# Optimization experiments

Hardware: AMD Instinct MI355X
Metric: run time of the kernel (lower is better)

## Reference

```python
import jax, jax.numpy as jnp
import numpy as np

N_EMBD = 1024
N_HEAD = 16
HEAD_DIM = N_EMBD // N_HEAD


def setup_inputs() -> dict:
    key = jax.random.key(0)
    k1, k2, k3 = jax.random.split(key, 3)
    x = jax.random.normal(k1, (4, 2048, N_EMBD), dtype=jnp.float32)
    w_qkv = jax.random.normal(k2, (N_EMBD, 3 * N_EMBD), dtype=jnp.float32) * (N_EMBD ** -0.5)
    w_proj = jax.random.normal(k3, (N_EMBD, N_EMBD), dtype=jnp.float32) * (N_EMBD ** -0.5)
    return {"x": x, "w_qkv": w_qkv, "w_proj": w_proj}


def reference(x, w_qkv, w_proj):
    B, T, C = x.shape
    qkv = jnp.einsum('btc,cd->btd', x, w_qkv)  # [B,T,3C]
    q, k, v = jnp.split(qkv, 3, axis=-1)
    def heads(t):
        return t.reshape(B, T, N_HEAD, HEAD_DIM).transpose(0, 2, 1, 3)  # [B,H,T,D]
    q, k, v = heads(q), heads(k), heads(v)
    scale = 1.0 / jnp.sqrt(jnp.asarray(HEAD_DIM, dtype=x.dtype))
    att = jnp.einsum('bhqd,bhkd->bhqk', q, k) * scale  # [B,H,T,T]
    causal = jnp.tril(jnp.ones((T, T), dtype=bool))
    att = jnp.where(causal[None, None], att, jnp.asarray(-jnp.inf, dtype=att.dtype))
    att = jax.nn.softmax(att, axis=-1)
    out = jnp.einsum('bhqk,bhkd->bhqd', att, v)  # [B,H,T,D]
    out = out.transpose(0, 2, 1, 3).reshape(B, T, C)
    return jnp.einsum('btc,cd->btd', out, w_proj)
```

## Files before the change

kernel.cpp:

```cpp
#include <hip/hip_runtime.h>
#include <cstdint>
#include <cstddef>
#include <type_traits>

typedef float  f32x4    __attribute__((ext_vector_type(4)));
typedef float  f32x16   __attribute__((ext_vector_type(16)));
typedef __bf16 bf16x8   __attribute__((ext_vector_type(8)));
typedef short  short4_t __attribute__((ext_vector_type(4)));
typedef short  short8_t __attribute__((ext_vector_type(8)));
typedef unsigned int uint4_t __attribute__((ext_vector_type(4)));

__device__ __forceinline__ short f2bf(float f) {
  return __builtin_bit_cast(short, (__bf16)f);
}

__device__ __forceinline__ unsigned pk2bf(float a, float b) {
  unsigned lo = (unsigned short)__builtin_bit_cast(unsigned short, f2bf(a));
  unsigned hi = (unsigned short)__builtin_bit_cast(unsigned short, f2bf(b));
  return lo | (hi << 16);
}

__device__ __forceinline__ void gl_lds16(const void* g, void* l) {
  __builtin_amdgcn_global_load_lds((const __attribute__((address_space(1))) void*)g,
                                   (__attribute__((address_space(3))) void*)l, 16, 0, 0);
}

__global__ void convert_bf16(const float* __restrict__ X, short* __restrict__ Xb) {
  int i = (blockIdx.x * 256 + threadIdx.x) * 4;
  f32x4 v = *(const f32x4*)&X[i];
  short4_t o;
#pragma unroll
  for (int j = 0; j < 4; j++) o[j] = f2bf(v[j]);
  *(short4_t*)&Xb[i] = o;
}

__global__ void transpose_bf16(const float* __restrict__ W, short* __restrict__ WT,
                               int K, int N) {
  __shared__ float tile[32][33];
  int tx = threadIdx.x & 31, ty = threadIdx.x >> 5;
  int n0 = blockIdx.x * 32, k0 = blockIdx.y * 32;
#pragma unroll
  for (int i = 0; i < 32; i += 8)
    tile[ty + i][tx] = W[(size_t)(k0 + ty + i) * N + n0 + tx];
  __syncthreads();
#pragma unroll
  for (int i = 0; i < 32; i += 8)
    WT[(size_t)(n0 + ty + i) * K + k0 + tx] = f2bf(tile[tx][ty + i]);
}

template <int MODE>
__global__ __launch_bounds__(256, 2) void gemm_bt(
    const short* __restrict__ A, const short* __restrict__ Bt,
    float* __restrict__ outf, short* __restrict__ Qo, short* __restrict__ Ko,
    short* __restrict__ Vo, int M, int N, int K) {
  __shared__ alignas(16) short As[128 * 32];
  __shared__ alignas(16) short Bs[128 * 32];
  const int tid = threadIdx.x;
  const int lane = tid & 63;
  const int g = lane & 15, q = lane >> 4;
  const int wave = tid >> 6;
  const int m0 = blockIdx.y * 128, n0 = blockIdx.x * 128;
  const int wm = (wave >> 1) * 64, wn = (wave & 1) * 64;

  const int srow = tid >> 2;
  const int scol = (tid & 3) * 8;
  const short* ap0 = A  + (size_t)(m0 + srow) * K + scol;
  const short* ap1 = A  + (size_t)(m0 + 64 + srow) * K + scol;
  const short* bp0 = Bt + (size_t)(n0 + srow) * K + scol;
  const short* bp1 = Bt + (size_t)(n0 + 64 + srow) * K + scol;
  short* la0 = &As[tid * 8];
  short* la1 = &As[(tid + 256) * 8];
  short* lb0 = &Bs[tid * 8];
  short* lb1 = &Bs[(tid + 256) * 8];

  f32x4 acc[4][4] = {};

  for (int k0 = 0; k0 < K; k0 += 32) {
    __syncthreads();
    gl_lds16(ap0 + k0, la0);
    gl_lds16(ap1 + k0, la1);
    gl_lds16(bp0 + k0, lb0);
    gl_lds16(bp1 + k0, lb1);
    __syncthreads();
    bf16x8 af[4], bfr[4];
#pragma unroll
    for (int mt = 0; mt < 4; mt++)
      af[mt] = *(const bf16x8*)&As[(wm + mt * 16 + g) * 32 + q * 8];
#pragma unroll
    for (int nt = 0; nt < 4; nt++)
      bfr[nt] = *(const bf16x8*)&Bs[(wn + nt * 16 + g) * 32 + q * 8];
#pragma unroll
    for (int mt = 0; mt < 4; mt++)
#pragma unroll
      for (int nt = 0; nt < 4; nt++)
        acc[mt][nt] = __builtin_amdgcn_mfma_f32_16x16x32_bf16(af[mt], bfr[nt],
                                                              acc[mt][nt], 0, 0, 0);
  }

  if (MODE == 0) {
#pragma unroll
    for (int mt = 0; mt < 4; mt++)
#pragma unroll
      for (int nt = 0; nt < 4; nt++) {
        int n = n0 + wn + nt * 16 + g;
        int mbase = m0 + wm + mt * 16 + q * 4;
#pragma unroll
        for (int r = 0; r < 4; r++)
          outf[(size_t)(mbase + r) * N + n] = acc[mt][nt][r];
      }
  } else {
#pragma unroll
    for (int nt = 0; nt < 4; nt++) {
      int n = n0 + wn + nt * 16 + g;
      int which = n >> 10;
      int c = n & 1023;
      int h = c >> 6, d = c & 63;
#pragma unroll
      for (int mt = 0; mt < 4; mt++) {
        int mbase = m0 + wm + mt * 16 + q * 4;
        int b = mbase >> 11, t = mbase & 2047;
        if (which == 2) {
          short4_t pv;
#pragma unroll
          for (int r = 0; r < 4; r++) pv[r] = f2bf(acc[mt][nt][r]);
          *(short4_t*)&Vo[((size_t)((b << 4) + h) * 64 + d) * 2048 + t] = pv;
        } else {
          short* dst = (which == 0) ? Qo : Ko;
#pragma unroll
          for (int r = 0; r < 4; r++)
            dst[((size_t)((b << 4) + h) * 2048 + (t + r)) * 64 + d] =
                f2bf(acc[mt][nt][r]);
        }
      }
    }
  }
}

__global__ __launch_bounds__(256, 2) void attn_fwd(
    const short* __restrict__ Qg, const short* __restrict__ Kg,
    const short* __restrict__ Vt, short* __restrict__ Og) {
  __shared__ alignas(16) short Ks[2][8192];
  __shared__ alignas(16) short Vs[2][8192];
  const int tid = threadIdx.x, lane = tid & 63, wave = tid >> 6;
  const int c = lane & 31;
  const int qh = lane >> 5;
  const int bh = blockIdx.x;
  const int b = bh >> 4, h = bh & 15;
  const size_t base = (size_t)bh * (2048 * 64);
  const float cs = 0.18033688011f;
  const int q_rel = wave * 32 + c;
  const int laneoff = (qh * 32 + c) * 8;

  const short* kp[4];
  const short* vp[4];
#pragma unroll
  for (int i = 0; i < 4; i++) {
    int u = i * 256 + tid;
    int uc = u & 31, uq = (u >> 5) & 1;
    kp[i] = Kg + base + (size_t)((u >> 8) * 32 + uc) * 64 + ((u >> 6) & 3) * 16 + uq * 8;
    vp[i] = Vt + base + (size_t)(((u >> 6) & 1) * 32 + uc) * 2048 + (u >> 7) * 16 + uq * 8;
  }

  auto stage = [&](int buf, int kt) {
    short* kd = &Ks[buf][tid * 8];
    short* vd = &Vs[buf][tid * 8];
#pragma unroll
    for (int i = 0; i < 4; i++) {
      gl_lds16(kp[i] + (size_t)kt * (128 * 64), kd + i * 2048);
      gl_lds16(vp[i] + (size_t)kt * 128, vd + i * 2048);
    }
  };

  int cur = 0;

  for (int half = 0; half < 2; half++) {
    const int qt = (half == 0) ? (int)blockIdx.y : 15 - (int)blockIdx.y;
    const int qrow = qt * 128 + wave * 32 + c;

    bf16x8 bq[4];
#pragma unroll
    for (int ks = 0; ks < 4; ks++) {
      bf16x8 v = *(const bf16x8*)&Qg[base + (size_t)qrow * 64 + ks * 16 + qh * 8];
#pragma unroll
      for (int j = 0; j < 8; j++) v[j] = (__bf16)((float)v[j] * cs);
      bq[ks] = v;
    }

    f32x16 ot[2] = {};
    float m_run = -1e30f, l_run = 0.0f;

    auto step = [&](auto diagc, const short* ksb, const short* vsb) {
      constexpr bool DIAG = decltype(diagc)::value;

      f32x16 st[4] = {};
      __builtin_amdgcn_s_setprio(1);
#pragma unroll
      for (int mt = 0; mt < 4; mt++)
#pragma unroll
        for (int ks = 0; ks < 4; ks++) {
          bf16x8 ak = *(const bf16x8*)&ksb[(mt * 4 + ks) * 512 + laneoff];
          st[mt] = __builtin_amdgcn_mfma_f32_32x32x16_bf16(ak, bq[ks],
                                                           st[mt], 0, 0, 0);
        }
      __builtin_amdgcn_s_setprio(0);

      float tm[4];
#pragma unroll
      for (int mt = 0; mt < 4; mt++) {
        float t = -1e30f;
#pragma unroll
        for (int r = 0; r < 16; r++) {
          if (DIAG) {
            int krel = mt * 32 + (r & 3) + 8 * (r >> 2) + 4 * qh;
            if (krel > q_rel) st[mt][r] = -1e30f;
          }
          t = fmaxf(t, st[mt][r]);
        }
        tm[mt] = t;
      }
      float tmax = fmaxf(fmaxf(tm[0], tm[1]), fmaxf(tm[2], tm[3]));
      tmax = fmaxf(tmax, __shfl_xor(tmax, 32));
      if (!__all(tmax - m_run <= 8.0f)) {
        const float mnew = fmaxf(m_run, tmax);
        const float alpha = __builtin_amdgcn_exp2f(m_run - mnew);
        l_run *= alpha;
#pragma unroll
        for (int mt = 0; mt < 2; mt++)
#pragma unroll
          for (int r = 0; r < 16; r++) ot[mt][r] *= alpha;
        m_run = mnew;
      }
      float ps[4];
#pragma unroll
      for (int mt = 0; mt < 4; mt++) {
        float s = 0.0f;
#pragma unroll
        for (int r = 0; r < 16; r++) {
          float p = __builtin_amdgcn_exp2f(st[mt][r] - m_run);
          s += p;
          st[mt][r] = p;
        }
        ps[mt] = s;
      }
      float psum = (ps[0] + ps[1]) + (ps[2] + ps[3]);
      psum += __shfl_xor(psum, 32);
      l_run += psum;

      __builtin_amdgcn_s_setprio(1);
#pragma unroll
      for (int kb = 0; kb < 8; kb++) {
        const int mt = kb >> 1, rb = (kb & 1) * 8;
        unsigned x0 = pk2bf(st[mt][rb + 0], st[mt][rb + 1]);
        unsigned x1 = pk2bf(st[mt][rb + 2], st[mt][rb + 3]);
        unsigned y0 = pk2bf(st[mt][rb + 4], st[mt][rb + 5]);
        unsigned y1 = pk2bf(st[mt][rb + 6], st[mt][rb + 7]);
        asm("v_permlane32_swap_b32 %0, %1" : "+v"(x0), "+v"(y0));
        asm("v_permlane32_swap_b32 %0, %1" : "+v"(x1), "+v"(y1));
        uint4_t pw;
        pw[0] = x0; pw[1] = x1; pw[2] = y0; pw[3] = y1;
        bf16x8 pb = __builtin_bit_cast(bf16x8, pw);
#pragma unroll
        for (int mtv = 0; mtv < 2; mtv++) {
          bf16x8 av = *(const bf16x8*)&vsb[(kb * 2 + mtv) * 512 + laneoff];
          ot[mtv] = __builtin_amdgcn_mfma_f32_32x32x16_bf16(av, pb,
                                                            ot[mtv], 0, 0, 0);
        }
      }
      __builtin_amdgcn_s_setprio(0);
    };

    __syncthreads();
    stage(cur, 0);
    for (int kt = 0; kt <= qt; kt++) {
      __syncthreads();
      if (kt < qt) stage(cur ^ 1, kt + 1);
      if (kt == qt)
        step(std::integral_constant<bool, true>{}, Ks[cur], Vs[cur]);
      else
        step(std::integral_constant<bool, false>{}, Ks[cur], Vs[cur]);
      cur ^= 1;
    }

    const float inv = 1.0f / l_run;
    const size_t obase = ((size_t)b * 2048 + qrow) * 1024 + h * 64 + qh * 4;
#pragma unroll
    for (int mt = 0; mt < 2; mt++)
#pragma unroll
      for (int rr = 0; rr < 4; rr++) {
        short4_t ov;
#pragma unroll
        for (int i = 0; i < 4; i++) ov[i] = f2bf(ot[mt][rr * 4 + i] * inv);
        *(short4_t*)&Og[obase + mt * 32 + rr * 8] = ov;
      }
  }
}

extern "C" void kernel_launch(void* const* d_in, const int* in_sizes, int n_in,
                              void* d_out, int out_size, void* d_ws, size_t ws_size,
                              hipStream_t stream) {
  const float* x      = (const float*)d_in[0];
  const float* w_qkv  = (const float*)d_in[1];
  const float* w_proj = (const float*)d_in[2];
  float* out = (float*)d_out;

  char* ws = (char*)d_ws;
  short* xb     = (short*)(ws);
  short* wqkvT  = (short*)(ws + 16777216);
  short* wprojT = (short*)(ws + 23068672);
  short* Qb     = (short*)(ws + 25165824);
  short* Kb     = (short*)(ws + 41943040);
  short* Vtb    = (short*)(ws + 58720256);

  convert_bf16<<<8192, 256, 0, stream>>>(x, xb);
  {
    dim3 gq(96, 32); transpose_bf16<<<gq, 256, 0, stream>>>(w_qkv, wqkvT, 1024, 3072);
    dim3 gp(32, 32); transpose_bf16<<<gp, 256, 0, stream>>>(w_proj, wprojT, 1024, 1024);
  }
  {
    dim3 g(24, 64);
    gemm_bt<1><<<g, 256, 0, stream>>>(xb, wqkvT, nullptr, Qb, Kb, Vtb, 8192, 3072, 1024);
  }
  {
    dim3 g(64, 8);
    attn_fwd<<<g, 256, 0, stream>>>(Qb, Kb, Vtb, xb );
  }
  {
    dim3 g(8, 64);
    gemm_bt<0><<<g, 256, 0, stream>>>(xb, wprojT, out, nullptr, nullptr, nullptr,
                                      8192, 1024, 1024);
  }
}
```

Before: 254.3 us.

## Add 256x256 double-buffered pipelined GEMM kernel for QKV projection

Replaces the 128x128 single-buffered QKV GEMM with a new 512-thread kernel that uses 256x256 tiles, K-step 64, double-buffered LDS filled by direct global-to-LDS loads, and fine-grained interleaving of loads with MFMA quadrants. It uses manual waitcnt, barriers and setprio, plus a block-index swizzle for L2 locality. The goal is to hide memory latency and raise MFMA utilisation in the largest GEMM. In exchange it uses much more LDS and many more registers, and it relies on delicate hand-written vmcnt accounting that could race if the counts are wrong.

```diff
diff --git a/kernel.cpp b/kernel.cpp
--- a/kernel.cpp
+++ b/kernel.cpp
@@ -48,11 +48,9 @@
     WT[(size_t)(n0 + ty + i) * K + k0 + tx] = f2bf(tile[tx][ty + i]);
 }
 
-template <int MODE>
 __global__ __launch_bounds__(256, 2) void gemm_bt(
     const short* __restrict__ A, const short* __restrict__ Bt,
-    float* __restrict__ outf, short* __restrict__ Qo, short* __restrict__ Ko,
-    short* __restrict__ Vo, int M, int N, int K) {
+    float* __restrict__ outf, int M, int N, int K) {
   __shared__ alignas(16) short As[128 * 32];
   __shared__ alignas(16) short Bs[128 * 32];
   const int tid = threadIdx.x;
@@ -97,40 +95,155 @@
                                                               acc[mt][nt], 0, 0, 0);
   }
 
-  if (MODE == 0) {
-#pragma unroll
-    for (int mt = 0; mt < 4; mt++)
-#pragma unroll
-      for (int nt = 0; nt < 4; nt++) {
-        int n = n0 + wn + nt * 16 + g;
-        int mbase = m0 + wm + mt * 16 + q * 4;
-#pragma unroll
-        for (int r = 0; r < 4; r++)
-          outf[(size_t)(mbase + r) * N + n] = acc[mt][nt][r];
-      }
-  } else {
+#pragma unroll
+  for (int mt = 0; mt < 4; mt++)
 #pragma unroll
     for (int nt = 0; nt < 4; nt++) {
       int n = n0 + wn + nt * 16 + g;
-      int which = n >> 10;
-      int c = n & 1023;
-      int h = c >> 6, d = c & 63;
-#pragma unroll
-      for (int mt = 0; mt < 4; mt++) {
-        int mbase = m0 + wm + mt * 16 + q * 4;
-        int b = mbase >> 11, t = mbase & 2047;
-        if (which == 2) {
-          short4_t pv;
-#pragma unroll
-          for (int r = 0; r < 4; r++) pv[r] = f2bf(acc[mt][nt][r]);
-          *(short4_t*)&Vo[((size_t)((b << 4) + h) * 64 + d) * 2048 + t] = pv;
-        } else {
-          short* dst = (which == 0) ? Qo : Ko;
-#pragma unroll
-          for (int r = 0; r < 4; r++)
-            dst[((size_t)((b << 4) + h) * 2048 + (t + r)) * 64 + d] =
-                f2bf(acc[mt][nt][r]);
-        }
+      int mbase = m0 + wm + mt * 16 + q * 4;
+#pragma unroll
+      for (int r = 0; r < 4; r++)
+        outf[(size_t)(mbase + r) * N + n] = acc[mt][nt][r];
+    }
+}
+
+__global__ __launch_bounds__(512, 2) void gemm256_qkv(
+    const short* __restrict__ A, const short* __restrict__ Bt,
+    short* __restrict__ Qo, short* __restrict__ Ko, short* __restrict__ Vo,
+    int M, int N, int K) {
+  __shared__ alignas(16) short As2[2][16384];
+  __shared__ alignas(16) short Bs2[2][16384];
+  const int tid = threadIdx.x;
+  const int lane = tid & 63;
+  const int g = lane & 15, q = lane >> 4;
+  const int wave = tid >> 6;
+  const int wr = wave >> 2, wc = wave & 3;
+
+  const int cpx = (gridDim.x * gridDim.y) >> 3;
+  const int lin = blockIdx.x + gridDim.x * blockIdx.y;
+  const int swz = (lin & 7) * cpx + (lin >> 3);
+  const int bx = swz % gridDim.x, by = swz / gridDim.x;
+  const int m0 = by * 256, n0 = bx * 256;
+
+  const int nkt = K >> 6;
+
+  const int srow  = (tid >> 7) * 16 + (tid & 15);
+  const int skoff = ((tid >> 6) & 1) * 32 + ((tid >> 4) & 3) * 8;
+
+  auto stA = [&](int buf, int h, int t) {
+    int tw = t & (nkt - 1);
+    const short* src = A + (size_t)(m0 + h * 128 + srow) * K + tw * 64 + skoff;
+    short* dst = &As2[buf][(h * 1024 + tid) * 8];
+    gl_lds16(src, dst);
+    gl_lds16(src + (size_t)64 * K, dst + 4096);
+  };
+  auto stB = [&](int buf, int h, int t) {
+    int tw = t & (nkt - 1);
+    const short* src = Bt + (size_t)(n0 + h * 128 + srow) * K + tw * 64 + skoff;
+    short* dst = &Bs2[buf][(h * 1024 + tid) * 8];
+    gl_lds16(src, dst);
+    gl_lds16(src + (size_t)64 * K, dst + 4096);
+  };
+
+  bf16x8 afr[4][2], bfr[4][2];
+  f32x4 acc[8][4] = {};
+
+  auto rdA = [&](int buf, int mh) {
+#pragma unroll
+    for (int mt = 0; mt < 4; mt++)
+#pragma unroll
+      for (int kk = 0; kk < 2; kk++)
+        afr[mt][kk] = *(const bf16x8*)
+            &As2[buf][(((wr * 8 + mh * 4 + mt) * 2 + kk) * 64 + lane) * 8];
+  };
+  auto rdB = [&](int buf, int nh) {
+#pragma unroll
+    for (int j = 0; j < 2; j++)
+#pragma unroll
+      for (int kk = 0; kk < 2; kk++)
+        bfr[nh * 2 + j][kk] = *(const bf16x8*)
+            &Bs2[buf][(((wc * 4 + nh * 2 + j) * 2 + kk) * 64 + lane) * 8];
+  };
+  auto quad = [&](int mh, int nh) {
+#pragma unroll
+    for (int kk = 0; kk < 2; kk++)
+#pragma unroll
+      for (int mt = 0; mt < 4; mt++)
+#pragma unroll
+        for (int j = 0; j < 2; j++)
+          acc[mh * 4 + mt][nh * 2 + j] = __builtin_amdgcn_mfma_f32_16x16x32_bf16(
+              afr[mt][kk], bfr[nh * 2 + j][kk], acc[mh * 4 + mt][nh * 2 + j], 0, 0, 0);
+  };
+  auto sync1 = [&]() {
+    asm volatile("s_waitcnt vmcnt(6)" ::: "memory");
+    __builtin_amdgcn_s_barrier();
+    asm volatile("s_waitcnt lgkmcnt(0)" ::: "memory");
+    __builtin_amdgcn_sched_barrier(0);
+    __builtin_amdgcn_s_setprio(1);
+  };
+  auto sync2 = [&]() {
+    __builtin_amdgcn_s_setprio(0);
+    __builtin_amdgcn_s_barrier();
+  };
+
+  stA(0, 0, 0);
+  stB(0, 1, 0);
+  stB(0, 0, 0);
+  stA(0, 1, 0);
+  stA(1, 0, 1);
+  stB(1, 1, 1);
+  asm volatile("s_waitcnt vmcnt(6)" ::: "memory");
+  __builtin_amdgcn_s_barrier();
+
+  const int niter = nkt >> 1;
+  for (int i = 0; i < niter; i++) {
+    const int t0 = 2 * i;
+    rdA(0, 0); rdB(0, 0);
+    stB(1, 0, t0 + 1);
+    sync1(); quad(0, 0); sync2();
+    rdB(0, 1);
+    stA(1, 1, t0 + 1);
+    sync1(); quad(0, 1); sync2();
+    rdA(0, 1);
+    stA(0, 0, t0 + 2);
+    sync1(); quad(1, 1); sync2();
+    stB(0, 1, t0 + 2);
+    sync1(); quad(1, 0); sync2();
+    rdA(1, 0); rdB(1, 0);
+    stB(0, 0, t0 + 2);
+    sync1(); quad(0, 0); sync2();
+    rdB(1, 1);
+    stA(0, 1, t0 + 2);
+    sync1(); quad(0, 1); sync2();
+    rdA(1, 1);
+    stA(1, 0, t0 + 3);
+    sync1(); quad(1, 1); sync2();
+    stB(1, 1, t0 + 3);
+    sync1(); quad(1, 0); sync2();
+  }
+  asm volatile("s_waitcnt vmcnt(0)" ::: "memory");
+
+#pragma unroll
+  for (int an = 0; an < 4; an++) {
+    int n = n0 + wc * 64 + an * 16 + g;
+    int which = n >> 10;
+    int cc = n & 1023;
+    int hh = cc >> 6, d = cc & 63;
+#pragma unroll
+    for (int am = 0; am < 8; am++) {
+      int mbase = m0 + wr * 128 + am * 16 + q * 4;
+      int b = mbase >> 11, t = mbase & 2047;
+      if (which == 2) {
+        short4_t pv;
+#pragma unroll
+        for (int r = 0; r < 4; r++) pv[r] = f2bf(acc[am][an][r]);
+        *(short4_t*)&Vo[((size_t)((b << 4) + hh) * 64 + d) * 2048 + t] = pv;
+      } else {
+        short* dst = (which == 0) ? Qo : Ko;
+#pragma unroll
+        for (int r = 0; r < 4; r++)
+          dst[((size_t)((b << 4) + hh) * 2048 + (t + r)) * 64 + d] =
+              f2bf(acc[am][an][r]);
       }
     }
   }
@@ -317,8 +430,8 @@
     dim3 gp(32, 32); transpose_bf16<<<gp, 256, 0, stream>>>(w_proj, wprojT, 1024, 1024);
   }
   {
-    dim3 g(24, 64);
-    gemm_bt<1><<<g, 256, 0, stream>>>(xb, wqkvT, nullptr, Qb, Kb, Vtb, 8192, 3072, 1024);
+    dim3 g(12, 32);
+    gemm256_qkv<<<g, 512, 0, stream>>>(xb, wqkvT, Qb, Kb, Vtb, 8192, 3072, 1024);
   }
   {
     dim3 g(64, 8);
@@ -326,7 +439,6 @@
   }
   {
     dim3 g(8, 64);
-    gemm_bt<0><<<g, 256, 0, stream>>>(xb, wprojT, out, nullptr, nullptr, nullptr,
-                                      8192, 1024, 1024);
-  }
-}
+    gemm_bt<<<g, 256, 0, stream>>>(xb, wprojT, out, 8192, 1024, 1024);
+  }
+}
```

Measured after the change: 279.5 us. +9.9%, slower.

## Double-buffer GEMM LDS tiles with fragment-ordered layout and block swizzle

Applied to the files above, without the earlier changes.

Replaces the single-buffered BK=32 GEMM with a double-buffered BK=64 version that prefetches the next K tile into the alternate LDS buffer while computing on the current one, needing one barrier per iteration instead of two. The LDS layout is rearranged so each lane reads its MFMA fragment contiguously, aiming to avoid bank conflicts. Block indices are swizzled across groups of 8 to improve cache locality across XCDs. LDS usage grows to 64KB per block, which may limit occupancy.

```diff
diff --git a/kernel.cpp b/kernel.cpp
--- a/kernel.cpp
+++ b/kernel.cpp
@@ -49,52 +49,74 @@
 }
 
 template <int MODE>
-__global__ __launch_bounds__(256, 2) void gemm_bt(
+__global__ __launch_bounds__(256, 2) void gemm_db(
     const short* __restrict__ A, const short* __restrict__ Bt,
     float* __restrict__ outf, short* __restrict__ Qo, short* __restrict__ Ko,
     short* __restrict__ Vo, int M, int N, int K) {
-  __shared__ alignas(16) short As[128 * 32];
-  __shared__ alignas(16) short Bs[128 * 32];
+  __shared__ alignas(16) short As[2][8192];
+  __shared__ alignas(16) short Bs[2][8192];
   const int tid = threadIdx.x;
   const int lane = tid & 63;
   const int g = lane & 15, q = lane >> 4;
   const int wave = tid >> 6;
-  const int m0 = blockIdx.y * 128, n0 = blockIdx.x * 128;
+
+  const int cpx = (gridDim.x * gridDim.y) >> 3;
+  const int lin = blockIdx.x + gridDim.x * blockIdx.y;
+  const int swz = (lin & 7) * cpx + (lin >> 3);
+  const int bx = swz % gridDim.x, by = swz / gridDim.x;
+  const int m0 = by * 128, n0 = bx * 128;
+
   const int wm = (wave >> 1) * 64, wn = (wave & 1) * 64;
-
-  const int srow = tid >> 2;
-  const int scol = (tid & 3) * 8;
-  const short* ap0 = A  + (size_t)(m0 + srow) * K + scol;
-  const short* ap1 = A  + (size_t)(m0 + 64 + srow) * K + scol;
-  const short* bp0 = Bt + (size_t)(n0 + srow) * K + scol;
-  const short* bp1 = Bt + (size_t)(n0 + 64 + srow) * K + scol;
-  short* la0 = &As[tid * 8];
-  short* la1 = &As[(tid + 256) * 8];
-  short* lb0 = &Bs[tid * 8];
-  short* lb1 = &Bs[(tid + 256) * 8];
+  const int wm4 = (wave >> 1) * 4, wn4 = (wave & 1) * 4;
+
+  const short* ap[4];
+  const short* bp[4];
+#pragma unroll
+  for (int i = 0; i < 4; i++) {
+    int u = i * 256 + tid;
+    int row = (u >> 7) * 16 + (u & 15);
+    int kc  = ((u >> 6) & 1) * 32 + ((u >> 4) & 3) * 8;
+    ap[i] = A  + (size_t)(m0 + row) * K + kc;
+    bp[i] = Bt + (size_t)(n0 + row) * K + kc;
+  }
+  auto stage = [&](int buf, int k0) {
+    short* ad = &As[buf][tid * 8];
+    short* bd = &Bs[buf][tid * 8];
+#pragma unroll
+    for (int i = 0; i < 4; i++) {
+      gl_lds16(ap[i] + k0, ad + i * 2048);
+      gl_lds16(bp[i] + k0, bd + i * 2048);
+    }
+  };
 
   f32x4 acc[4][4] = {};
-
-  for (int k0 = 0; k0 < K; k0 += 32) {
+  const int nk = K >> 6;
+  int cur = 0;
+
+  stage(0, 0);
+  for (int kt = 0; kt < nk; kt++) {
     __syncthreads();
-    gl_lds16(ap0 + k0, la0);
-    gl_lds16(ap1 + k0, la1);
-    gl_lds16(bp0 + k0, lb0);
-    gl_lds16(bp1 + k0, lb1);
-    __syncthreads();
-    bf16x8 af[4], bfr[4];
+    if (kt + 1 < nk) stage(cur ^ 1, (kt + 1) << 6);
+    bf16x8 af[4][2], bfr[4][2];
 #pragma unroll
     for (int mt = 0; mt < 4; mt++)
-      af[mt] = *(const bf16x8*)&As[(wm + mt * 16 + g) * 32 + q * 8];
+#pragma unroll
+      for (int kk = 0; kk < 2; kk++)
+        af[mt][kk] = *(const bf16x8*)&As[cur][(((wm4 + mt) * 2 + kk) * 64 + lane) * 8];
 #pragma unroll
     for (int nt = 0; nt < 4; nt++)
-      bfr[nt] = *(const bf16x8*)&Bs[(wn + nt * 16 + g) * 32 + q * 8];
-#pragma unroll
-    for (int mt = 0; mt < 4; mt++)
-#pragma unroll
-      for (int nt = 0; nt < 4; nt++)
-        acc[mt][nt] = __builtin_amdgcn_mfma_f32_16x16x32_bf16(af[mt], bfr[nt],
-                                                              acc[mt][nt], 0, 0, 0);
+#pragma unroll
+      for (int kk = 0; kk < 2; kk++)
+        bfr[nt][kk] = *(const bf16x8*)&Bs[cur][(((wn4 + nt) * 2 + kk) * 64 + lane) * 8];
+#pragma unroll
+    for (int kk = 0; kk < 2; kk++)
+#pragma unroll
+      for (int mt = 0; mt < 4; mt++)
+#pragma unroll
+        for (int nt = 0; nt < 4; nt++)
+          acc[mt][nt] = __builtin_amdgcn_mfma_f32_16x16x32_bf16(af[mt][kk],
+                            bfr[nt][kk], acc[mt][nt], 0, 0, 0);
+    cur ^= 1;
   }
 
   if (MODE == 0) {
@@ -113,8 +135,8 @@
     for (int nt = 0; nt < 4; nt++) {
       int n = n0 + wn + nt * 16 + g;
       int which = n >> 10;
-      int c = n & 1023;
-      int h = c >> 6, d = c & 63;
+      int cc = n & 1023;
+      int h = cc >> 6, d = cc & 63;
 #pragma unroll
       for (int mt = 0; mt < 4; mt++) {
         int mbase = m0 + wm + mt * 16 + q * 4;
@@ -318,7 +340,7 @@
   }
   {
     dim3 g(24, 64);
-    gemm_bt<1><<<g, 256, 0, stream>>>(xb, wqkvT, nullptr, Qb, Kb, Vtb, 8192, 3072, 1024);
+    gemm_db<1><<<g, 256, 0, stream>>>(xb, wqkvT, nullptr, Qb, Kb, Vtb, 8192, 3072, 1024);
   }
   {
     dim3 g(64, 8);
@@ -326,7 +348,7 @@
   }
   {
     dim3 g(8, 64);
-    gemm_bt<0><<<g, 256, 0, stream>>>(xb, wprojT, out, nullptr, nullptr, nullptr,
+    gemm_db<0><<<g, 256, 0, stream>>>(xb, wprojT, out, nullptr, nullptr, nullptr,
                                       8192, 1024, 1024);
   }
 }
```

Measured after the change: 293.6 us. 1.15x slower.

## Use BK=64 fragment-ordered LDS tiles and XCD-aware block swizzle in GEMMs

Applied to the files above, without the earlier changes.

Splits the templated GEMM into a QKV GEMM with a 64-deep K step and a projection GEMM. The QKV GEMM stages A and B into shared memory in a fragment-major order, so each lane reads its MFMA operands contiguously, and it halves the number of barrier pairs per K. Both GEMMs remap block indices so consecutive blocks spread across the 8 XCDs and neighbouring tiles share L2. The QKV kernel doubles its LDS use while declaring occupancy 4, which may limit how many blocks actually fit per CU.

```diff
diff --git a/kernel.cpp b/kernel.cpp
--- a/kernel.cpp
+++ b/kernel.cpp
@@ -48,18 +48,21 @@
     WT[(size_t)(n0 + ty + i) * K + k0 + tx] = f2bf(tile[tx][ty + i]);
 }
 
-template <int MODE>
-__global__ __launch_bounds__(256, 2) void gemm_bt(
+__global__ __launch_bounds__(256, 2) void gemm_proj(
     const short* __restrict__ A, const short* __restrict__ Bt,
-    float* __restrict__ outf, short* __restrict__ Qo, short* __restrict__ Ko,
-    short* __restrict__ Vo, int M, int N, int K) {
+    float* __restrict__ outf, int M, int N, int K) {
   __shared__ alignas(16) short As[128 * 32];
   __shared__ alignas(16) short Bs[128 * 32];
   const int tid = threadIdx.x;
   const int lane = tid & 63;
   const int g = lane & 15, q = lane >> 4;
   const int wave = tid >> 6;
-  const int m0 = blockIdx.y * 128, n0 = blockIdx.x * 128;
+
+  const int cpx = (gridDim.x * gridDim.y) >> 3;
+  const int lin = blockIdx.x + gridDim.x * blockIdx.y;
+  const int w = (lin & 7) * cpx + (lin >> 3);
+  const int m0 = (w / gridDim.x) * 128, n0 = (w % gridDim.x) * 128;
+
   const int wm = (wave >> 1) * 64, wn = (wave & 1) * 64;
 
   const int srow = tid >> 2;
@@ -97,40 +100,106 @@
                                                               acc[mt][nt], 0, 0, 0);
   }
 
-  if (MODE == 0) {
-#pragma unroll
-    for (int mt = 0; mt < 4; mt++)
-#pragma unroll
-      for (int nt = 0; nt < 4; nt++) {
-        int n = n0 + wn + nt * 16 + g;
-        int mbase = m0 + wm + mt * 16 + q * 4;
-#pragma unroll
-        for (int r = 0; r < 4; r++)
-          outf[(size_t)(mbase + r) * N + n] = acc[mt][nt][r];
-      }
-  } else {
+#pragma unroll
+  for (int mt = 0; mt < 4; mt++)
 #pragma unroll
     for (int nt = 0; nt < 4; nt++) {
       int n = n0 + wn + nt * 16 + g;
-      int which = n >> 10;
-      int c = n & 1023;
-      int h = c >> 6, d = c & 63;
-#pragma unroll
-      for (int mt = 0; mt < 4; mt++) {
-        int mbase = m0 + wm + mt * 16 + q * 4;
-        int b = mbase >> 11, t = mbase & 2047;
-        if (which == 2) {
-          short4_t pv;
-#pragma unroll
-          for (int r = 0; r < 4; r++) pv[r] = f2bf(acc[mt][nt][r]);
-          *(short4_t*)&Vo[((size_t)((b << 4) + h) * 64 + d) * 2048 + t] = pv;
-        } else {
-          short* dst = (which == 0) ? Qo : Ko;
-#pragma unroll
-          for (int r = 0; r < 4; r++)
-            dst[((size_t)((b << 4) + h) * 2048 + (t + r)) * 64 + d] =
-                f2bf(acc[mt][nt][r]);
-        }
+      int mbase = m0 + wm + mt * 16 + q * 4;
+#pragma unroll
+      for (int r = 0; r < 4; r++)
+        outf[(size_t)(mbase + r) * N + n] = acc[mt][nt][r];
+    }
+}
+
+__global__ __launch_bounds__(256, 4) void gemm_bk64(
+    const short* __restrict__ A, const short* __restrict__ Bt,
+    short* __restrict__ Qo, short* __restrict__ Ko, short* __restrict__ Vo,
+    int M, int N, int K) {
+  __shared__ alignas(16) short As[8192];
+  __shared__ alignas(16) short Bs[8192];
+  const int tid = threadIdx.x;
+  const int lane = tid & 63;
+  const int g = lane & 15, q = lane >> 4;
+  const int wave = tid >> 6;
+
+  const int cpx = (gridDim.x * gridDim.y) >> 3;
+  const int lin = blockIdx.x + gridDim.x * blockIdx.y;
+  const int w = (lin & 7) * cpx + (lin >> 3);
+  const int m0 = (w / gridDim.x) * 128, n0 = (w % gridDim.x) * 128;
+
+  const int wm = (wave >> 1) * 64, wn = (wave & 1) * 64;
+  const int wm4 = (wave >> 1) * 4, wn4 = (wave & 1) * 4;
+
+  const short* ap[4];
+  const short* bp[4];
+#pragma unroll
+  for (int i = 0; i < 4; i++) {
+    int u = i * 256 + tid;
+    int row = (u >> 7) * 16 + (u & 15);
+    int kc  = ((u >> 6) & 1) * 32 + ((u >> 4) & 3) * 8;
+    ap[i] = A  + (size_t)(m0 + row) * K + kc;
+    bp[i] = Bt + (size_t)(n0 + row) * K + kc;
+  }
+
+  f32x4 acc[4][4] = {};
+  const int nk = K >> 6;
+
+  for (int kt = 0; kt < nk; kt++) {
+    const int k0 = kt << 6;
+    __syncthreads();
+    {
+      short* ad = &As[tid * 8];
+      short* bd = &Bs[tid * 8];
+#pragma unroll
+      for (int i = 0; i < 4; i++) {
+        gl_lds16(ap[i] + k0, ad + i * 2048);
+        gl_lds16(bp[i] + k0, bd + i * 2048);
+      }
+    }
+    __syncthreads();
+    bf16x8 af[4][2], bfr[4][2];
+#pragma unroll
+    for (int mt = 0; mt < 4; mt++)
+#pragma unroll
+      for (int kk = 0; kk < 2; kk++)
+        af[mt][kk] = *(const bf16x8*)&As[(((wm4 + mt) * 2 + kk) * 64 + lane) * 8];
+#pragma unroll
+    for (int nt = 0; nt < 4; nt++)
+#pragma unroll
+      for (int kk = 0; kk < 2; kk++)
+        bfr[nt][kk] = *(const bf16x8*)&Bs[(((wn4 + nt) * 2 + kk) * 64 + lane) * 8];
+#pragma unroll
+    for (int kk = 0; kk < 2; kk++)
+#pragma unroll
+      for (int mt = 0; mt < 4; mt++)
+#pragma unroll
+        for (int nt = 0; nt < 4; nt++)
+          acc[mt][nt] = __builtin_amdgcn_mfma_f32_16x16x32_bf16(af[mt][kk],
+                            bfr[nt][kk], acc[mt][nt], 0, 0, 0);
+  }
+
+#pragma unroll
+  for (int nt = 0; nt < 4; nt++) {
+    int n = n0 + wn + nt * 16 + g;
+    int which = n >> 10;
+    int cc = n & 1023;
+    int h = cc >> 6, d = cc & 63;
+#pragma unroll
+    for (int mt = 0; mt < 4; mt++) {
+      int mbase = m0 + wm + mt * 16 + q * 4;
+      int b = mbase >> 11, t = mbase & 2047;
+      if (which == 2) {
+        short4_t pv;
+#pragma unroll
+        for (int r = 0; r < 4; r++) pv[r] = f2bf(acc[mt][nt][r]);
+        *(short4_t*)&Vo[((size_t)((b << 4) + h) * 64 + d) * 2048 + t] = pv;
+      } else {
+        short* dst = (which == 0) ? Qo : Ko;
+#pragma unroll
+        for (int r = 0; r < 4; r++)
+          dst[((size_t)((b << 4) + h) * 2048 + (t + r)) * 64 + d] =
+              f2bf(acc[mt][nt][r]);
       }
     }
   }
@@ -318,7 +387,7 @@
   }
   {
     dim3 g(24, 64);
-    gemm_bt<1><<<g, 256, 0, stream>>>(xb, wqkvT, nullptr, Qb, Kb, Vtb, 8192, 3072, 1024);
+    gemm_bk64<<<g, 256, 0, stream>>>(xb, wqkvT, Qb, Kb, Vtb, 8192, 3072, 1024);
   }
   {
     dim3 g(64, 8);
@@ -326,7 +395,6 @@
   }
   {
     dim3 g(8, 64);
-    gemm_bt<0><<<g, 256, 0, stream>>>(xb, wprojT, out, nullptr, nullptr, nullptr,
-                                      8192, 1024, 1024);
-  }
-}
+    gemm_proj<<<g, 256, 0, stream>>>(xb, wprojT, out, 8192, 1024, 1024);
+  }
+}
```

Result: slower. 284.4 us (+11.9%).
